# Kernel optimization log

Hardware: AMD Instinct MI355X
Metric: run time of the kernel (lower is better)

## Reference

```python
import jax, jax.numpy as jnp
import numpy as np


def setup_inputs() -> dict:
    key = jax.random.key(0)
    k1, k2 = jax.random.split(key)
    N, D = 65536, 512
    feeds = jax.random.normal(k1, (N, D), dtype=jnp.float32)
    feeds_repeat_times = jax.random.randint(k2, (N,), 0, 8)
    return {
        "feeds": feeds,
        "feeds_repeat_times": feeds_repeat_times,
        "output_feeds_size": 262144,
    }


def reference(feeds, feeds_repeat_times, output_feeds_size):
    # Equivalent of the per-row repeat + cat + pad + truncate, as one fused gather.
    # Output row j comes from source row i where cumsum(repeats) first exceeds j.
    cum = jnp.cumsum(feeds_repeat_times)          # [N]
    total = cum[-1]                               # total repeated rows
    pos = jnp.arange(output_feeds_size)           # [S]
    idx = jnp.searchsorted(cum, pos, side="right")  # source row per output row
    valid = pos < total                           # rows beyond total are zero pad
    idx = jnp.clip(idx, 0, feeds.shape[0] - 1)
    out = jnp.where(valid[:, None], feeds[idx], jnp.zeros((), dtype=feeds.dtype))
    return out
```

## Files before the change

### kernel.cpp

```cpp
#include <hip/hip_runtime.h>

#define NROWS 65536
#define DCOLS 512
#define D4    128
#define CHUNK 256
#define NCHUNK (NROWS / CHUNK)

typedef float f32x4 __attribute__((ext_vector_type(4)));


__global__ __launch_bounds__(256) void chunk_sum_kernel(const int* __restrict__ rep,
                                                        int* __restrict__ chunksum) {
    const int b = blockIdx.x;
    const int t = threadIdx.x;
    int v = rep[b * CHUNK + t];
#pragma unroll
    for (int off = 32; off; off >>= 1) v += __shfl_down(v, off);
    __shared__ int ws4[4];
    if ((t & 63) == 0) ws4[t >> 6] = v;
    __syncthreads();
    if (t == 0) chunksum[b] = ws4[0] + ws4[1] + ws4[2] + ws4[3];
}

__global__ __launch_bounds__(256) void scan_chunks_kernel(const int* __restrict__ chunksum,
                                                          int* __restrict__ chunkoff,
                                                          int* __restrict__ totalp) {
    __shared__ int s[NCHUNK];
    const int t = threadIdx.x;
    const int v = chunksum[t];
    s[t] = v;
    __syncthreads();
    for (int off = 1; off < NCHUNK; off <<= 1) {
        int add = (t >= off) ? s[t - off] : 0;
        __syncthreads();
        s[t] += add;
        __syncthreads();
    }
    chunkoff[t] = s[t] - v;
    if (t == NCHUNK - 1) totalp[0] = s[t];
}

__global__ __launch_bounds__(256) void build_idx_kernel(const int* __restrict__ rep,
                                                        const int* __restrict__ chunkoff,
                                                        unsigned short* __restrict__ idx16,
                                                        int S) {
    const int b = blockIdx.x;
    const int t = threadIdx.x;
    const int i = b * CHUNK + t;
    const int r = rep[i];
    __shared__ int s[CHUNK];
    s[t] = r;
    __syncthreads();
    for (int off = 1; off < CHUNK; off <<= 1) {
        int add = (t >= off) ? s[t - off] : 0;
        __syncthreads();
        s[t] += add;
        __syncthreads();
    }
    int end = chunkoff[b] + s[t];
    const int start = end - r;
    if (start >= S) return;
    if (end > S) end = S;
    for (int j = start; j < end; ++j) idx16[j] = (unsigned short)i;
}

__global__ __launch_bounds__(256) void gather_kernel(const f32x4* __restrict__ feeds,
                                                     const unsigned short* __restrict__ idx16,
                                                     const int* __restrict__ totalp,
                                                     f32x4* __restrict__ out,
                                                     int S) {
    int bid = blockIdx.x;
    const int cpx = gridDim.x >> 3;
    bid = (bid & 7) * cpx + (bid >> 3);

    const int wave = bid * 4 + (threadIdx.x >> 6);
    const int lane = threadIdx.x & 63;
    const int j0 = wave * 4;
    if (j0 >= S) return;

    const int total = totalp[0];

    f32x4 a[4], b[4];
#pragma unroll
    for (int q = 0; q < 4; ++q) {
        const int j = j0 + q;
        if (j < total) {
            const int si = idx16[j];
            const f32x4* src = feeds + (long long)si * D4;
            a[q] = src[lane];
            b[q] = src[lane + 64];
        } else {
            a[q] = (f32x4)0.f;
            b[q] = (f32x4)0.f;
        }
    }
#pragma unroll
    for (int q = 0; q < 4; ++q) {
        f32x4* dst = out + (long long)(j0 + q) * D4;
        dst[lane]      = a[q];
        dst[lane + 64] = b[q];
    }
}

extern "C" void kernel_launch(void* const* d_in, const int* in_sizes, int n_in,
                              void* d_out, int out_size, void* d_ws, size_t ws_size,
                              hipStream_t stream) {
    const float* feeds = (const float*)d_in[0];
    const int*   rep   = (const int*)d_in[1];
    const int S = out_size / DCOLS;

    int* ws       = (int*)d_ws;
    int* chunksum = ws;
    int* chunkoff = ws + 256;
    int* totalp   = ws + 512;
    unsigned short* idx16 = (unsigned short*)(ws + 1024);

    chunk_sum_kernel<<<NCHUNK, CHUNK, 0, stream>>>(rep, chunksum);
    scan_chunks_kernel<<<1, NCHUNK, 0, stream>>>(chunksum, chunkoff, totalp);
    build_idx_kernel<<<NCHUNK, CHUNK, 0, stream>>>(rep, chunkoff, idx16, S);
    gather_kernel<<<S / 16, 256, 0, stream>>>((const f32x4*)feeds, idx16, totalp,
                                              (f32x4*)d_out, S);
}
```

Measured before the change: 620.4 us.

## Fuse three-kernel prefix scan into one kernel computing chunk offsets redundantly

The separate chunk-sum, chunk-scan and index-build kernels are replaced by one kernel. Each block recomputes its exclusive prefix by summing all preceding repeat counts itself, which removes two launches and their dependencies. In exchange it does redundant work: total reads are O(N²/CHUNK), up to about 65K ints for the last block. The gather's address arithmetic is also narrowed from 64-bit to 32-bit unsigned offsets.

```diff
diff --git a/kernel.cpp b/kernel.cpp
--- a/kernel.cpp
+++ b/kernel.cpp
@@ -9,43 +9,22 @@
 typedef float f32x4 __attribute__((ext_vector_type(4)));
 
 
-__global__ __launch_bounds__(256) void chunk_sum_kernel(const int* __restrict__ rep,
-                                                        int* __restrict__ chunksum) {
+__global__ __launch_bounds__(256) void scan_idx_kernel(const int* __restrict__ rep,
+                                                       unsigned short* __restrict__ idx16,
+                                                       int* __restrict__ totalp,
+                                                       int S) {
     const int b = blockIdx.x;
     const int t = threadIdx.x;
-    int v = rep[b * CHUNK + t];
+
+    int part = 0;
+    for (int k = t; k < b * CHUNK; k += CHUNK) part += rep[k];
 #pragma unroll
-    for (int off = 32; off; off >>= 1) v += __shfl_down(v, off);
-    __shared__ int ws4[4];
-    if ((t & 63) == 0) ws4[t >> 6] = v;
+    for (int off = 32; off; off >>= 1) part += __shfl_down(part, off);
+    __shared__ int wsum[4];
+    if ((t & 63) == 0) wsum[t >> 6] = part;
     __syncthreads();
-    if (t == 0) chunksum[b] = ws4[0] + ws4[1] + ws4[2] + ws4[3];
-}
+    const int ex = wsum[0] + wsum[1] + wsum[2] + wsum[3];
 
-__global__ __launch_bounds__(256) void scan_chunks_kernel(const int* __restrict__ chunksum,
-                                                          int* __restrict__ chunkoff,
-                                                          int* __restrict__ totalp) {
-    __shared__ int s[NCHUNK];
-    const int t = threadIdx.x;
-    const int v = chunksum[t];
-    s[t] = v;
-    __syncthreads();
-    for (int off = 1; off < NCHUNK; off <<= 1) {
-        int add = (t >= off) ? s[t - off] : 0;
-        __syncthreads();
-        s[t] += add;
-        __syncthreads();
-    }
-    chunkoff[t] = s[t] - v;
-    if (t == NCHUNK - 1) totalp[0] = s[t];
-}
-
-__global__ __launch_bounds__(256) void build_idx_kernel(const int* __restrict__ rep,
-                                                        const int* __restrict__ chunkoff,
-                                                        unsigned short* __restrict__ idx16,
-                                                        int S) {
-    const int b = blockIdx.x;
-    const int t = threadIdx.x;
     const int i = b * CHUNK + t;
     const int r = rep[i];
     __shared__ int s[CHUNK];
@@ -57,7 +36,9 @@
         s[t] += add;
         __syncthreads();
     }
-    int end = chunkoff[b] + s[t];
+    int end = ex + s[t];
+    if (i == NROWS - 1) totalp[0] = end;
+
     const int start = end - r;
     if (start >= S) return;
     if (end > S) end = S;
@@ -86,7 +67,7 @@
         const int j = j0 + q;
         if (j < total) {
             const int si = idx16[j];
-            const f32x4* src = feeds + (long long)si * D4;
+            const f32x4* src = feeds + (unsigned)(si * D4);
             a[q] = src[lane];
             b[q] = src[lane + 64];
         } else {
@@ -109,15 +90,11 @@
     const int*   rep   = (const int*)d_in[1];
     const int S = out_size / DCOLS;
 
-    int* ws       = (int*)d_ws;
-    int* chunksum = ws;
-    int* chunkoff = ws + 256;
-    int* totalp   = ws + 512;
-    unsigned short* idx16 = (unsigned short*)(ws + 1024);
+    int* ws     = (int*)d_ws;
+    int* totalp = ws;
+    unsigned short* idx16 = (unsigned short*)(ws + 64);
 
-    chunk_sum_kernel<<<NCHUNK, CHUNK, 0, stream>>>(rep, chunksum);
-    scan_chunks_kernel<<<1, NCHUNK, 0, stream>>>(chunksum, chunkoff, totalp);
-    build_idx_kernel<<<NCHUNK, CHUNK, 0, stream>>>(rep, chunkoff, idx16, S);
+    scan_idx_kernel<<<NCHUNK, CHUNK, 0, stream>>>(rep, idx16, totalp, S);
     gather_kernel<<<S / 16, 256, 0, stream>>>((const f32x4*)feeds, idx16, totalp,
                                               (f32x4*)d_out, S);
 }
```

Measured after the change: 676.0 us. 9.0% more time.
